# Optimization experiments

Measured on AMD Instinct MI355X. Metric: run time of the kernel, lower is better.

## Reference

```python
import jax, jax.numpy as jnp
import numpy as np

N = 100000   # total nodes (types a: [0,50000), b: [50000,100000))
E = 500000   # edges per edge type
T = 4        # number of edge types
D_IN = 128
H = 4        # heads
F = 32       # out_feats per head
NEG_SLOPE = 0.2


def setup_inputs() -> dict:
    key = jax.random.key(0)
    ks = jax.random.split(key, 8)
    feat = jax.random.normal(ks[0], (N, D_IN), dtype=jnp.float32)
    src = jax.random.randint(ks[1], (T, E), 0, N)
    dst = jax.random.randint(ks[2], (T, E), 0, N)
    is_b = jnp.arange(N) >= (N // 2)  # node-type mask (type2mask)
    W = jax.random.normal(ks[3], (T, D_IN, H * F), dtype=jnp.float32) * (1.0 / np.sqrt(D_IN))
    attn_l = jax.random.normal(ks[4], (T, H, F), dtype=jnp.float32) * 0.1
    attn_r = jax.random.normal(ks[5], (T, H, F), dtype=jnp.float32) * 0.1
    W_merge = jax.random.normal(ks[6], (2 * H * F, F), dtype=jnp.float32) * (1.0 / np.sqrt(2 * H * F))
    b_merge = jax.random.normal(ks[7], (F,), dtype=jnp.float32) * 0.01
    return {"feat": feat, "src": src, "dst": dst, "is_b": is_b,
            "W": W, "attn_l": attn_l, "attn_r": attn_r,
            "W_merge": W_merge, "b_merge": b_merge}


def _gat_etype(feat, src_t, dst_t, W_t, al_t, ar_t):
    # Projected features: [N, H, F]
    ft = (feat @ W_t).reshape(N, H, F)
    el = jnp.einsum('nhf,hf->nh', ft, al_t)  # [N, H]
    er = jnp.einsum('nhf,hf->nh', ft, ar_t)  # [N, H]
    # u_add_v then LeakyReLU: [E, H]
    e = el[src_t] + er[dst_t]
    e = jnp.where(e > 0, e, NEG_SLOPE * e)
    # edge_softmax over incoming edges of each dst node (stable)
    m = jax.lax.stop_gradient(jax.ops.segment_max(e, dst_t, num_segments=N))
    ex = jnp.exp(e - m[dst_t])
    denom = jax.ops.segment_sum(ex, dst_t, num_segments=N)
    a = ex / denom[dst_t]  # [E, H]
    # u_mul_e + scatter-sum: [N, H, F]
    msg = ft[src_t] * a[:, :, None]
    out = jax.ops.segment_sum(msg, dst_t, num_segments=N)
    return out.reshape(N, H * F)


def reference(feat, src, dst, is_b, W, attn_l, attn_r, W_merge, b_merge):
    outs = [_gat_etype(feat, src[t], dst[t], W[t], attn_l[t], attn_r[t])
            for t in range(T)]
    # etypes dst order: a, a, b, b -> two per-etype feats per dst ntype
    feat_a = jnp.concatenate([outs[0], outs[1]], axis=1) @ W_merge + b_merge  # [N, F]
    feat_b = jnp.concatenate([outs[2], outs[3]], axis=1) @ W_merge + b_merge  # [N, F]
    # base_aggr_func: start with type-a result, overwrite type-b rows
    return jnp.where(is_b[:, None], feat_b, feat_a)
```

## Files before the change

kernel.cpp:

```cpp
#include <hip/hip_runtime.h>

typedef short short8 __attribute__((ext_vector_type(8)));
typedef float f32x4 __attribute__((ext_vector_type(4)));

#define N_NODES 100000
#define N_A     50000
#define N_EDGES 500000
#define N_T     4
#define D_IN    128
#define HF      128
#define BCOLS   144
#define TN      (N_T * N_NODES)
#define TE      (N_T * N_EDGES)
#define NB1     ((TN + 1023) / 1024)
#define TILE_E  (BCOLS * D_IN)

__device__ __forceinline__ unsigned short f2b(float f) {
  unsigned int u = __float_as_uint(f);
  u += 0x7FFFu + ((u >> 16) & 1u);
  return (unsigned short)(u >> 16);
}
__device__ __forceinline__ unsigned int pk2(float lo, float hi) {
  return (unsigned int)f2b(lo) | ((unsigned int)f2b(hi) << 16);
}
__device__ __forceinline__ float blo(unsigned int u) { return __uint_as_float(u << 16); }
__device__ __forceinline__ float bhi(unsigned int u) { return __uint_as_float(u & 0xFFFF0000u); }
__device__ __forceinline__ float lrelu_exp(float e) {
  return __expf(e > 0.f ? e : 0.2f * e);
}

__global__ __launch_bounds__(256) void k_prepB(const float* __restrict__ W,
    const float* __restrict__ al, const float* __restrict__ ar,
    unsigned short* __restrict__ Bt)
{
  int idx = blockIdx.x * 256 + threadIdx.x;
  if (idx >= N_T * D_IN) return;
  int t = idx >> 7, k = idx & 127;
  const float* Wr = W + ((size_t)t * D_IN + k) * HF;
  unsigned short* o = Bt + (size_t)t * TILE_E;
  for (int j = 0; j < HF; ++j)
    o[(j * D_IN + k) ^ ((j & 7) << 3)] = f2b(Wr[j]);
  for (int h = 0; h < 4; ++h) {
    float sl = 0.f, sr = 0.f;
    const float* alh = al + (t * 4 + h) * 32;
    const float* arh = ar + (t * 4 + h) * 32;
    for (int f = 0; f < 32; ++f) { float w = Wr[h * 32 + f]; sl += w * alh[f]; sr += w * arh[f]; }
    int jl = 128 + h, jr = 132 + h;
    o[(jl * D_IN + k) ^ ((jl & 7) << 3)] = f2b(sl);
    o[(jr * D_IN + k) ^ ((jr & 7) << 3)] = f2b(sr);
  }
  for (int j = 136; j < 144; ++j)
    o[(j * D_IN + k) ^ ((j & 7) << 3)] = 0;
}

__global__ __launch_bounds__(256) void k_prepWm(const float* __restrict__ Wm,
    unsigned short* __restrict__ WmT)
{
  int idx = blockIdx.x * 256 + threadIdx.x;
  if (idx >= 256 * 32) return;
  int kidx = idx >> 5, j = idx & 31;
  int slot = kidx >> 7, p = kidx & 127;
  int col = (p & 7) * 16 + (p >> 3);
  WmT[j * 256 + kidx] = f2b(Wm[(slot * 128 + col) * 32 + j]);
}

__global__ __launch_bounds__(256, 4) void k_proj(const float* __restrict__ feat,
    const unsigned short* __restrict__ Btg,
    unsigned short* __restrict__ ftg,
    float* __restrict__ elg, float* __restrict__ erg)
{
  __shared__ __align__(16) unsigned short Bs[TILE_E];
  const int tid = threadIdx.x;
  const int wave = tid >> 6, lane = tid & 63;
  const int l15 = lane & 15, g = lane >> 4;
  const int wrow0 = blockIdx.x * 64 + wave * 16;

  short8 a[4];
  {
    int row = wrow0 + l15;
    const float* fr = feat + (size_t)(row < N_NODES ? row : N_NODES - 1) * D_IN;
#pragma unroll
    for (int kt = 0; kt < 4; ++kt) {
      float4 v0 = *(const float4*)(fr + kt * 32 + g * 8);
      float4 v1 = *(const float4*)(fr + kt * 32 + g * 8 + 4);
      short8 s;
      s[0] = (short)f2b(v0.x); s[1] = (short)f2b(v0.y);
      s[2] = (short)f2b(v0.z); s[3] = (short)f2b(v0.w);
      s[4] = (short)f2b(v1.x); s[5] = (short)f2b(v1.y);
      s[6] = (short)f2b(v1.z); s[7] = (short)f2b(v1.w);
      a[kt] = s;
    }
  }

  for (int t = 0; t < N_T; ++t) {
    if (t > 0) __syncthreads();
    {
      const uint4* src = (const uint4*)(Btg + (size_t)t * TILE_E);
      uint4* dstv = (uint4*)Bs;
#pragma unroll
      for (int i = 0; i < 9; ++i)
        dstv[i * 256 + tid] = src[i * 256 + tid];
    }
    __syncthreads();

    f32x4 acc[8];
#pragma unroll
    for (int ct = 0; ct < 8; ++ct) {
      f32x4 c = {0.f, 0.f, 0.f, 0.f};
#pragma unroll
      for (int kt = 0; kt < 4; ++kt) {
        int row = ct * 16 + l15;
        int boff = (row * 256 + kt * 64 + g * 16) ^ ((l15 & 7) << 4);
        short8 b = *(const short8*)((const char*)Bs + boff);
        c = __builtin_amdgcn_mfma_f32_16x16x32_bf16(a[kt], b, c, 0, 0, 0);
      }
      acc[ct] = c;
    }
    {
      f32x4 c8 = {0.f, 0.f, 0.f, 0.f};
#pragma unroll
      for (int kt = 0; kt < 4; ++kt) {
        int row = 128 + l15;
        int boff = (row * 256 + kt * 64 + g * 16) ^ ((l15 & 7) << 4);
        short8 b = *(const short8*)((const char*)Bs + boff);
        c8 = __builtin_amdgcn_mfma_f32_16x16x32_bf16(a[kt], b, c8, 0, 0, 0);
      }
      if (l15 < 8) {
#pragma unroll
        for (int r = 0; r < 4; ++r) {
          int row = wrow0 + g * 4 + r;
          if (row < N_NODES) {
            float v = c8[r];
            if (l15 < 4) elg[((size_t)t * N_NODES + row) * 4 + l15] = v;
            else         erg[((size_t)t * N_NODES + row) * 4 + (l15 - 4)] = v;
          }
        }
      }
    }
#pragma unroll
    for (int r = 0; r < 4; ++r) {
      int row = wrow0 + g * 4 + r;
      if (row < N_NODES) {
        uint4 o;
        o.x = pk2(acc[0][r], acc[1][r]);
        o.y = pk2(acc[2][r], acc[3][r]);
        o.z = pk2(acc[4][r], acc[5][r]);
        o.w = pk2(acc[6][r], acc[7][r]);
        *(uint4*)(ftg + ((size_t)t * N_NODES + row) * HF + l15 * 8) = o;
      }
    }
  }
}

__global__ __launch_bounds__(256) void k_hist(const int* __restrict__ dst,
    int* __restrict__ cnt, int* __restrict__ rank) {
  int idx = blockIdx.x * 256 + threadIdx.x;
  if (idx >= TE) return;
  int t = idx / N_EDGES;
  int d = dst[idx];
  bool keep = (t < 2) ? (d < N_A) : (d >= N_A);
  if (keep) rank[idx] = atomicAdd(&cnt[t * N_NODES + d], 1);
}

__global__ __launch_bounds__(256) void k_scan1(const int* __restrict__ cnt,
    int* __restrict__ ofs, int* __restrict__ bsum) {
  __shared__ int ts[256];
  int b = blockIdx.x, t = threadIdx.x;
  int base = b * 1024 + t * 4;
  int v0 = 0, v1 = 0, v2 = 0, v3 = 0;
  if (base + 0 < TN) v0 = cnt[base + 0];
  if (base + 1 < TN) v1 = cnt[base + 1];
  if (base + 2 < TN) v2 = cnt[base + 2];
  if (base + 3 < TN) v3 = cnt[base + 3];
  int s = v0 + v1 + v2 + v3;
  ts[t] = s;
  __syncthreads();
  for (int o = 1; o < 256; o <<= 1) {
    int x = (t >= o) ? ts[t - o] : 0;
    __syncthreads();
    ts[t] += x;
    __syncthreads();
  }
  int run = ts[t] - s;
  if (base + 0 < TN) ofs[base + 0] = run; run += v0;
  if (base + 1 < TN) ofs[base + 1] = run; run += v1;
  if (base + 2 < TN) ofs[base + 2] = run; run += v2;
  if (base + 3 < TN) ofs[base + 3] = run;
  if (t == 255) bsum[b] = ts[255];
}

__global__ __launch_bounds__(512) void k_scan2(int* __restrict__ bsum) {
  __shared__ int ts[512];
  int t = threadIdx.x;
  int v = (t < NB1) ? bsum[t] : 0;
  ts[t] = v;
  __syncthreads();
  for (int o = 1; o < 512; o <<= 1) {
    int x = (t >= o) ? ts[t - o] : 0;
    __syncthreads();
    ts[t] += x;
    __syncthreads();
  }
  if (t < NB1) bsum[t] = ts[t] - v;
}

__global__ __launch_bounds__(256) void k_scatter(const int* __restrict__ src, const int* __restrict__ dst,
    const int* __restrict__ ofs, const int* __restrict__ bsum, const int* __restrict__ rank,
    int* __restrict__ bkt) {
  int idx = blockIdx.x * 256 + threadIdx.x;
  if (idx >= TE) return;
  int t = idx / N_EDGES;
  int d = dst[idx];
  bool keep = (t < 2) ? (d < N_A) : (d >= N_A);
  if (!keep) return;
  int key = t * N_NODES + d;
  int p = ofs[key] + bsum[key >> 10] + rank[idx];
  bkt[p] = t * N_NODES + src[idx];
}

__global__ __launch_bounds__(256) void k_gather(const int* __restrict__ bkt,
    const int* __restrict__ ofs, const int* __restrict__ cnt, const int* __restrict__ bsum,
    const float* __restrict__ elg, const float* __restrict__ erg,
    const uint4* __restrict__ ftu, uint4* __restrict__ aggb)
{
  int wid = blockIdx.x * 4 + (threadIdx.x >> 6);
  int lane = threadIdx.x & 63;
  int g = lane >> 4, l15 = lane & 15;
  int pid = wid * 4 + g;
  int n = pid >> 1, slot = pid & 1;
  int t = slot + ((n >= N_A) ? 2 : 0);
  int key = t * N_NODES + n;
  int base = ofs[key] + bsum[key >> 10];
  int c = cnt[key];
  float4 er4 = *(const float4*)(erg + (size_t)key * 4);
  float a0 = 0.f, a1 = 0.f, a2 = 0.f, a3 = 0.f, a4 = 0.f, a5 = 0.f, a6 = 0.f, a7 = 0.f;
  float d0 = 0.f, d1 = 0.f, d2 = 0.f, d3 = 0.f;
  int i = 0;
  for (; i + 1 < c; i += 2) {
    int s0 = bkt[base + i];
    int s1 = bkt[base + i + 1];
    float4 el0 = *(const float4*)(elg + (size_t)s0 * 4);
    float4 el1 = *(const float4*)(elg + (size_t)s1 * 4);
    uint4 u0 = ftu[(size_t)s0 * 16 + l15];
    uint4 u1 = ftu[(size_t)s1 * 16 + l15];
    float w0 = lrelu_exp(el0.x + er4.x);
    float w1 = lrelu_exp(el0.y + er4.y);
    float w2 = lrelu_exp(el0.z + er4.z);
    float w3 = lrelu_exp(el0.w + er4.w);
    d0 += w0; d1 += w1; d2 += w2; d3 += w3;
    a0 += w0 * blo(u0.x); a1 += w0 * bhi(u0.x);
    a2 += w1 * blo(u0.y); a3 += w1 * bhi(u0.y);
    a4 += w2 * blo(u0.z); a5 += w2 * bhi(u0.z);
    a6 += w3 * blo(u0.w); a7 += w3 * bhi(u0.w);
    w0 = lrelu_exp(el1.x + er4.x);
    w1 = lrelu_exp(el1.y + er4.y);
    w2 = lrelu_exp(el1.z + er4.z);
    w3 = lrelu_exp(el1.w + er4.w);
    d0 += w0; d1 += w1; d2 += w2; d3 += w3;
    a0 += w0 * blo(u1.x); a1 += w0 * bhi(u1.x);
    a2 += w1 * blo(u1.y); a3 += w1 * bhi(u1.y);
    a4 += w2 * blo(u1.z); a5 += w2 * bhi(u1.z);
    a6 += w3 * blo(u1.w); a7 += w3 * bhi(u1.w);
  }
  if (i < c) {
    int s0 = bkt[base + i];
    float4 el0 = *(const float4*)(elg + (size_t)s0 * 4);
    uint4 u0 = ftu[(size_t)s0 * 16 + l15];
    float w0 = lrelu_exp(el0.x + er4.x);
    float w1 = lrelu_exp(el0.y + er4.y);
    float w2 = lrelu_exp(el0.z + er4.z);
    float w3 = lrelu_exp(el0.w + er4.w);
    d0 += w0; d1 += w1; d2 += w2; d3 += w3;
    a0 += w0 * blo(u0.x); a1 += w0 * bhi(u0.x);
    a2 += w1 * blo(u0.y); a3 += w1 * bhi(u0.y);
    a4 += w2 * blo(u0.z); a5 += w2 * bhi(u0.z);
    a6 += w3 * blo(u0.w); a7 += w3 * bhi(u0.w);
  }
  float i0 = (c > 0) ? 1.f / d0 : 0.f;
  float i1 = (c > 0) ? 1.f / d1 : 0.f;
  float i2 = (c > 0) ? 1.f / d2 : 0.f;
  float i3 = (c > 0) ? 1.f / d3 : 0.f;
  uint4 o;
  o.x = pk2(a0 * i0, a1 * i0);
  o.y = pk2(a2 * i1, a3 * i1);
  o.z = pk2(a4 * i2, a5 * i2);
  o.w = pk2(a6 * i3, a7 * i3);
  aggb[(size_t)n * 32 + slot * 16 + l15] = o;
}

__global__ __launch_bounds__(256) void k_merge(const unsigned short* __restrict__ aggb,
    const unsigned short* __restrict__ WmT, const float* __restrict__ bm,
    float* __restrict__ out)
{
  __shared__ __align__(16) unsigned short Al[64 * 264];
  __shared__ __align__(16) unsigned short Bl[32 * 264];
  int n0 = blockIdx.x * 64;
  int tid = threadIdx.x;
  const uint4* asrc = (const uint4*)(aggb + (size_t)n0 * 256);
  for (int i = tid; i < 2048; i += 256) {
    int r = i >> 5, c = i & 31;
    *(uint4*)&Al[r * 264 + c * 8] = asrc[r * 32 + c];
  }
  for (int i = tid; i < 1024; i += 256) {
    int r = i >> 5, c = i & 31;
    *(uint4*)&Bl[r * 264 + c * 8] = ((const uint4*)WmT)[r * 32 + c];
  }
  __syncthreads();
  int wave = tid >> 6, lane = tid & 63;
  int l15 = lane & 15, lk = (lane >> 4) * 8;
  short8 a[8];
#pragma unroll
  for (int kt = 0; kt < 8; ++kt)
    a[kt] = *(const short8*)&Al[(wave * 16 + l15) * 264 + kt * 32 + lk];
  f32x4 acc0 = {0.f, 0.f, 0.f, 0.f}, acc1 = {0.f, 0.f, 0.f, 0.f};
#pragma unroll
  for (int kt = 0; kt < 8; ++kt) {
    short8 b0 = *(const short8*)&Bl[l15 * 264 + kt * 32 + lk];
    short8 b1 = *(const short8*)&Bl[(16 + l15) * 264 + kt * 32 + lk];
    acc0 = __builtin_amdgcn_mfma_f32_16x16x32_bf16(a[kt], b0, acc0, 0, 0, 0);
    acc1 = __builtin_amdgcn_mfma_f32_16x16x32_bf16(a[kt], b1, acc1, 0, 0, 0);
  }
  float bm0 = bm[l15], bm1 = bm[16 + l15];
#pragma unroll
  for (int r = 0; r < 4; ++r) {
    int row = n0 + wave * 16 + (lane >> 4) * 4 + r;
    if (row < N_NODES) {
      out[(size_t)row * 32 + l15] = acc0[r] + bm0;
      out[(size_t)row * 32 + 16 + l15] = acc1[r] + bm1;
    }
  }
}

extern "C" void kernel_launch(void* const* d_in, const int* in_sizes, int n_in,
                              void* d_out, int out_size, void* d_ws, size_t ws_size,
                              hipStream_t stream)
{
  const float* feat = (const float*)d_in[0];
  const int*   src  = (const int*)d_in[1];
  const int*   dst  = (const int*)d_in[2];
  const float* W    = (const float*)d_in[4];
  const float* al   = (const float*)d_in[5];
  const float* ar   = (const float*)d_in[6];
  const float* Wm   = (const float*)d_in[7];
  const float* bm   = (const float*)d_in[8];
  float* out = (float*)d_out;
  (void)in_sizes; (void)n_in; (void)out_size; (void)ws_size;

  char* w = (char*)d_ws;
  size_t o = 0;
  auto take = [&](size_t bytes) -> void* {
    void* p = w + o;
    o += (bytes + 255) & ~(size_t)255;
    return p;
  };
  unsigned short* Btg = (unsigned short*)take((size_t)N_T * TILE_E * 2);
  unsigned short* WmT = (unsigned short*)take((size_t)32 * 256 * 2);
  unsigned short* ftg = (unsigned short*)take((size_t)N_T * N_NODES * HF * 2);
  float* elg   = (float*)take((size_t)N_T * N_NODES * 4 * 4);
  float* erg   = (float*)take((size_t)N_T * N_NODES * 4 * 4);
  int*   cntb  = (int*)take((size_t)TN * 4);
  int*   ofs   = (int*)take((size_t)TN * 4);
  int*   bsum  = (int*)take(4096);
  int*   rank  = (int*)take((size_t)TE * 4);
  int*   bkt   = (int*)take((size_t)TE * 4);
  unsigned short* aggb = (unsigned short*)take((size_t)(N_NODES + 64) * 256 * 2);

  hipMemsetAsync(cntb, 0, (size_t)TN * 4, stream);

  k_prepB<<<2, 256, 0, stream>>>(W, al, ar, Btg);
  k_prepWm<<<32, 256, 0, stream>>>(Wm, WmT);
  k_proj<<<1563, 256, 0, stream>>>(feat, Btg, ftg, elg, erg);
  k_hist<<<(TE + 255) / 256, 256, 0, stream>>>(dst, cntb, rank);
  k_scan1<<<NB1, 256, 0, stream>>>(cntb, ofs, bsum);
  k_scan2<<<1, 512, 0, stream>>>(bsum);
  k_scatter<<<(TE + 255) / 256, 256, 0, stream>>>(src, dst, ofs, bsum, rank, bkt);
  k_gather<<<12500, 256, 0, stream>>>(bkt, ofs, cntb, bsum, elg, erg, (const uint4*)ftg, (uint4*)aggb);
  k_merge<<<1563, 256, 0, stream>>>(aggb, WmT, bm, out);
}
```

Before: 202.0 us.

## Merge prep kernels, widen proj blocks, halve gather lanes per node, use exp2

```diff
diff --git a/kernel.cpp b/kernel.cpp
--- a/kernel.cpp
+++ b/kernel.cpp
@@ -14,6 +14,7 @@
 #define TE      (N_T * N_EDGES)
 #define NB1     ((TN + 1023) / 1024)
 #define TILE_E  (BCOLS * D_IN)
+#define LOG2E   1.44269504088896340736f
 
 __device__ __forceinline__ unsigned short f2b(float f) {
   unsigned int u = __float_as_uint(f);
@@ -25,46 +26,40 @@
 }
 __device__ __forceinline__ float blo(unsigned int u) { return __uint_as_float(u << 16); }
 __device__ __forceinline__ float bhi(unsigned int u) { return __uint_as_float(u & 0xFFFF0000u); }
-__device__ __forceinline__ float lrelu_exp(float e) {
-  return __expf(e > 0.f ? e : 0.2f * e);
-}
-
-__global__ __launch_bounds__(256) void k_prepB(const float* __restrict__ W,
+
+__global__ __launch_bounds__(256) void k_prep(const float* __restrict__ W,
     const float* __restrict__ al, const float* __restrict__ ar,
-    unsigned short* __restrict__ Bt)
-{
-  int idx = blockIdx.x * 256 + threadIdx.x;
-  if (idx >= N_T * D_IN) return;
-  int t = idx >> 7, k = idx & 127;
-  const float* Wr = W + ((size_t)t * D_IN + k) * HF;
-  unsigned short* o = Bt + (size_t)t * TILE_E;
-  for (int j = 0; j < HF; ++j)
-    o[(j * D_IN + k) ^ ((j & 7) << 3)] = f2b(Wr[j]);
-  for (int h = 0; h < 4; ++h) {
-    float sl = 0.f, sr = 0.f;
-    const float* alh = al + (t * 4 + h) * 32;
-    const float* arh = ar + (t * 4 + h) * 32;
-    for (int f = 0; f < 32; ++f) { float w = Wr[h * 32 + f]; sl += w * alh[f]; sr += w * arh[f]; }
-    int jl = 128 + h, jr = 132 + h;
-    o[(jl * D_IN + k) ^ ((jl & 7) << 3)] = f2b(sl);
-    o[(jr * D_IN + k) ^ ((jr & 7) << 3)] = f2b(sr);
-  }
-  for (int j = 136; j < 144; ++j)
-    o[(j * D_IN + k) ^ ((j & 7) << 3)] = 0;
-}
-
-__global__ __launch_bounds__(256) void k_prepWm(const float* __restrict__ Wm,
-    unsigned short* __restrict__ WmT)
-{
-  int idx = blockIdx.x * 256 + threadIdx.x;
-  if (idx >= 256 * 32) return;
-  int kidx = idx >> 5, j = idx & 31;
-  int slot = kidx >> 7, p = kidx & 127;
-  int col = (p & 7) * 16 + (p >> 3);
-  WmT[j * 256 + kidx] = f2b(Wm[(slot * 128 + col) * 32 + j]);
-}
-
-__global__ __launch_bounds__(256, 4) void k_proj(const float* __restrict__ feat,
+    const float* __restrict__ Wm,
+    unsigned short* __restrict__ Bt, unsigned short* __restrict__ WmT)
+{
+  if (blockIdx.x < 2) {
+    int idx = blockIdx.x * 256 + threadIdx.x;
+    int t = idx >> 7, k = idx & 127;
+    const float* Wr = W + ((size_t)t * D_IN + k) * HF;
+    unsigned short* o = Bt + (size_t)t * TILE_E;
+    for (int j = 0; j < HF; ++j)
+      o[(j * D_IN + k) ^ ((j & 7) << 3)] = f2b(Wr[j]);
+    for (int h = 0; h < 4; ++h) {
+      float sl = 0.f, sr = 0.f;
+      const float* alh = al + (t * 4 + h) * 32;
+      const float* arh = ar + (t * 4 + h) * 32;
+      for (int f = 0; f < 32; ++f) { float w = Wr[h * 32 + f]; sl += w * alh[f]; sr += w * arh[f]; }
+      int jl = 128 + h, jr = 132 + h;
+      o[(jl * D_IN + k) ^ ((jl & 7) << 3)] = f2b(sl * LOG2E);
+      o[(jr * D_IN + k) ^ ((jr & 7) << 3)] = f2b(sr * LOG2E);
+    }
+    for (int j = 136; j < 144; ++j)
+      o[(j * D_IN + k) ^ ((j & 7) << 3)] = 0;
+  } else {
+    int idx = (blockIdx.x - 2) * 256 + threadIdx.x;
+    int kidx = idx >> 5, j = idx & 31;
+    int slot = kidx >> 7, p = kidx & 127;
+    int col = (p & 7) * 16 + (p >> 3);
+    WmT[j * 256 + kidx] = f2b(Wm[(slot * 128 + col) * 32 + j]);
+  }
+}
+
+__global__ __launch_bounds__(512, 8) void k_proj(const float* __restrict__ feat,
     const unsigned short* __restrict__ Btg,
     unsigned short* __restrict__ ftg,
     float* __restrict__ elg, float* __restrict__ erg)
@@ -73,7 +68,7 @@
   const int tid = threadIdx.x;
   const int wave = tid >> 6, lane = tid & 63;
   const int l15 = lane & 15, g = lane >> 4;
-  const int wrow0 = blockIdx.x * 64 + wave * 16;
+  const int wrow0 = blockIdx.x * 128 + wave * 16;
 
   short8 a[4];
   {
@@ -97,9 +92,8 @@
     {
       const uint4* src = (const uint4*)(Btg + (size_t)t * TILE_E);
       uint4* dstv = (uint4*)Bs;
-#pragma unroll
-      for (int i = 0; i < 9; ++i)
-        dstv[i * 256 + tid] = src[i * 256 + tid];
+      for (int i = tid; i < 2304; i += 512)
+        dstv[i] = src[i];
     }
     __syncthreads();
 
@@ -225,67 +219,92 @@
 {
   int wid = blockIdx.x * 4 + (threadIdx.x >> 6);
   int lane = threadIdx.x & 63;
-  int g = lane >> 4, l15 = lane & 15;
-  int pid = wid * 4 + g;
+  int g8 = lane >> 3, l7 = lane & 7;
+  int pid = wid * 8 + g8;
   int n = pid >> 1, slot = pid & 1;
   int t = slot + ((n >= N_A) ? 2 : 0);
   int key = t * N_NODES + n;
   int base = ofs[key] + bsum[key >> 10];
   int c = cnt[key];
   float4 er4 = *(const float4*)(erg + (size_t)key * 4);
-  float a0 = 0.f, a1 = 0.f, a2 = 0.f, a3 = 0.f, a4 = 0.f, a5 = 0.f, a6 = 0.f, a7 = 0.f;
+  float a00 = 0.f, a01 = 0.f, a02 = 0.f, a03 = 0.f, a04 = 0.f, a05 = 0.f, a06 = 0.f, a07 = 0.f;
+  float a10 = 0.f, a11 = 0.f, a12 = 0.f, a13 = 0.f, a14 = 0.f, a15 = 0.f, a16 = 0.f, a17 = 0.f;
   float d0 = 0.f, d1 = 0.f, d2 = 0.f, d3 = 0.f;
+  int qb = l7 * 2;
   int i = 0;
   for (; i + 1 < c; i += 2) {
     int s0 = bkt[base + i];
     int s1 = bkt[base + i + 1];
     float4 el0 = *(const float4*)(elg + (size_t)s0 * 4);
     float4 el1 = *(const float4*)(elg + (size_t)s1 * 4);
-    uint4 u0 = ftu[(size_t)s0 * 16 + l15];
-    uint4 u1 = ftu[(size_t)s1 * 16 + l15];
-    float w0 = lrelu_exp(el0.x + er4.x);
-    float w1 = lrelu_exp(el0.y + er4.y);
-    float w2 = lrelu_exp(el0.z + er4.z);
-    float w3 = lrelu_exp(el0.w + er4.w);
+    uint4 u0a = ftu[(size_t)s0 * 16 + qb];
+    uint4 u0b = ftu[(size_t)s0 * 16 + qb + 1];
+    uint4 u1a = ftu[(size_t)s1 * 16 + qb];
+    uint4 u1b = ftu[(size_t)s1 * 16 + qb + 1];
+    float s, w0, w1, w2, w3;
+    s = el0.x + er4.x; w0 = exp2f(fmaxf(s, 0.2f * s));
+    s = el0.y + er4.y; w1 = exp2f(fmaxf(s, 0.2f * s));
+    s = el0.z + er4.z; w2 = exp2f(fmaxf(s, 0.2f * s));
+    s = el0.w + er4.w; w3 = exp2f(fmaxf(s, 0.2f * s));
     d0 += w0; d1 += w1; d2 += w2; d3 += w3;
-    a0 += w0 * blo(u0.x); a1 += w0 * bhi(u0.x);
-    a2 += w1 * blo(u0.y); a3 += w1 * bhi(u0.y);
-    a4 += w2 * blo(u0.z); a5 += w2 * bhi(u0.z);
-    a6 += w3 * blo(u0.w); a7 += w3 * bhi(u0.w);
-    w0 = lrelu_exp(el1.x + er4.x);
-    w1 = lrelu_exp(el1.y + er4.y);
-    w2 = lrelu_exp(el1.z + er4.z);
-    w3 = lrelu_exp(el1.w + er4.w);
+    a00 += w0 * blo(u0a.x); a01 += w0 * bhi(u0a.x);
+    a02 += w1 * blo(u0a.y); a03 += w1 * bhi(u0a.y);
+    a04 += w2 * blo(u0a.z); a05 += w2 * bhi(u0a.z);
+    a06 += w3 * blo(u0a.w); a07 += w3 * bhi(u0a.w);
+    a10 += w0 * blo(u0b.x); a11 += w0 * bhi(u0b.x);
+    a12 += w1 * blo(u0b.y); a13 += w1 * bhi(u0b.y);
+    a14 += w2 * blo(u0b.z); a15 += w2 * bhi(u0b.z);
+    a16 += w3 * blo(u0b.w); a17 += w3 * bhi(u0b.w);
+    s = el1.x + er4.x; w0 = exp2f(fmaxf(s, 0.2f * s));
+    s = el1.y + er4.y; w1 = exp2f(fmaxf(s, 0.2f * s));
+    s = el1.z + er4.z; w2 = exp2f(fmaxf(s, 0.2f * s));
+    s = el1.w + er4.w; w3 = exp2f(fmaxf(s, 0.2f * s));
     d0 += w0; d1 += w1; d2 += w2; d3 += w3;
-    a0 += w0 * blo(u1.x); a1 += w0 * bhi(u1.x);
-    a2 += w1 * blo(u1.y); a3 += w1 * bhi(u1.y);
-    a4 += w2 * blo(u1.z); a5 += w2 * bhi(u1.z);
-    a6 += w3 * blo(u1.w); a7 += w3 * bhi(u1.w);
+    a00 += w0 * blo(u1a.x); a01 += w0 * bhi(u1a.x);
+    a02 += w1 * blo(u1a.y); a03 += w1 * bhi(u1a.y);
+    a04 += w2 * blo(u1a.z); a05 += w2 * bhi(u1a.z);
+    a06 += w3 * blo(u1a.w); a07 += w3 * bhi(u1a.w);
+    a10 += w0 * blo(u1b.x); a11 += w0 * bhi(u1b.x);
+    a12 += w1 * blo(u1b.y); a13 += w1 * bhi(u1b.y);
+    a14 += w2 * blo(u1b.z); a15 += w2 * bhi(u1b.z);
+    a16 += w3 * blo(u1b.w); a17 += w3 * bhi(u1b.w);
   }
   if (i < c) {
     int s0 = bkt[base + i];
     float4 el0 = *(const float4*)(elg + (size_t)s0 * 4);
-    uint4 u0 = ftu[(size_t)s0 * 16 + l15];
-    float w0 = lrelu_exp(el0.x + er4.x);
-    float w1 = lrelu_exp(el0.y + er4.y);
-    float w2 = lrelu_exp(el0.z + er4.z);
-    float w3 = lrelu_exp(el0.w + er4.w);
+    uint4 u0a = ftu[(size_t)s0 * 16 + qb];
+    uint4 u0b = ftu[(size_t)s0 * 16 + qb + 1];
+    float s, w0, w1, w2, w3;
+    s = el0.x + er4.x; w0 = exp2f(fmaxf(s, 0.2f * s));
+    s = el0.y + er4.y; w1 = exp2f(fmaxf(s, 0.2f * s));
+    s = el0.z + er4.z; w2 = exp2f(fmaxf(s, 0.2f * s));
+    s = el0.w + er4.w; w3 = exp2f(fmaxf(s, 0.2f * s));
     d0 += w0; d1 += w1; d2 += w2; d3 += w3;
-    a0 += w0 * blo(u0.x); a1 += w0 * bhi(u0.x);
-    a2 += w1 * blo(u0.y); a3 += w1 * bhi(u0.y);
-    a4 += w2 * blo(u0.z); a5 += w2 * bhi(u0.z);
-    a6 += w3 * blo(u0.w); a7 += w3 * bhi(u0.w);
+    a00 += w0 * blo(u0a.x); a01 += w0 * bhi(u0a.x);
+    a02 += w1 * blo(u0a.y); a03 += w1 * bhi(u0a.y);
+    a04 += w2 * blo(u0a.z); a05 += w2 * bhi(u0a.z);
+    a06 += w3 * blo(u0a.w); a07 += w3 * bhi(u0a.w);
+    a10 += w0 * blo(u0b.x); a11 += w0 * bhi(u0b.x);
+    a12 += w1 * blo(u0b.y); a13 += w1 * bhi(u0b.y);
+    a14 += w2 * blo(u0b.z); a15 += w2 * bhi(u0b.z);
+    a16 += w3 * blo(u0b.w); a17 += w3 * bhi(u0b.w);
   }
   float i0 = (c > 0) ? 1.f / d0 : 0.f;
   float i1 = (c > 0) ? 1.f / d1 : 0.f;
   float i2 = (c > 0) ? 1.f / d2 : 0.f;
   float i3 = (c > 0) ? 1.f / d3 : 0.f;
-  uint4 o;
-  o.x = pk2(a0 * i0, a1 * i0);
-  o.y = pk2(a2 * i1, a3 * i1);
-  o.z = pk2(a4 * i2, a5 * i2);
-  o.w = pk2(a6 * i3, a7 * i3);
-  aggb[(size_t)n * 32 + slot * 16 + l15] = o;
+  uint4 oA, oB;
+  oA.x = pk2(a00 * i0, a01 * i0);
+  oA.y = pk2(a02 * i1, a03 * i1);
+  oA.z = pk2(a04 * i2, a05 * i2);
+  oA.w = pk2(a06 * i3, a07 * i3);
+  oB.x = pk2(a10 * i0, a11 * i0);
+  oB.y = pk2(a12 * i1, a13 * i1);
+  oB.z = pk2(a14 * i2, a15 * i2);
+  oB.w = pk2(a16 * i3, a17 * i3);
+  size_t ob = (size_t)n * 32 + slot * 16 + qb;
+  aggb[ob] = oA;
+  aggb[ob + 1] = oB;
 }
 
 __global__ __launch_bounds__(256) void k_merge(const unsigned short* __restrict__ aggb,
@@ -367,13 +386,12 @@
 
   hipMemsetAsync(cntb, 0, (size_t)TN * 4, stream);
 
-  k_prepB<<<2, 256, 0, stream>>>(W, al, ar, Btg);
-  k_prepWm<<<32, 256, 0, stream>>>(Wm, WmT);
-  k_proj<<<1563, 256, 0, stream>>>(feat, Btg, ftg, elg, erg);
+  k_prep<<<34, 256, 0, stream>>>(W, al, ar, Wm, Btg, WmT);
+  k_proj<<<782, 512, 0, stream>>>(feat, Btg, ftg, elg, erg);
   k_hist<<<(TE + 255) / 256, 256, 0, stream>>>(dst, cntb, rank);
   k_scan1<<<NB1, 256, 0, stream>>>(cntb, ofs, bsum);
   k_scan2<<<1, 512, 0, stream>>>(bsum);
   k_scatter<<<(TE + 255) / 256, 256, 0, stream>>>(src, dst, ofs, bsum, rank, bkt);
-  k_gather<<<12500, 256, 0, stream>>>(bkt, ofs, cntb, bsum, elg, erg, (const uint4*)ftg, (uint4*)aggb);
+  k_gather<<<6250, 256, 0, stream>>>(bkt, ofs, cntb, bsum, elg, erg, (const uint4*)ftg, (uint4*)aggb);
   k_merge<<<1563, 256, 0, stream>>>(aggb, WmT, bm, out);
 }
```

After: 293.1 us. 1.45x slower.
